# Performance work log

Hardware: AMD Instinct MI355X
Metric: run time of the kernel (lower is better)

The kernel has to match this reference:

```python
import jax, jax.numpy as jnp
import numpy as np

N = 100000   # nodes
E = 800000   # edges
H = 256      # hidden_dim == input_dim
L = 3        # num_layers
G = 64       # graphs in batch


def setup_inputs() -> dict:
    key = jax.random.key(0)
    ks = jax.random.split(key, 16)
    s = 0.05
    inp = {
        'x': jax.random.normal(ks[0], (N, H), jnp.float32),
        'edge_index': jax.random.randint(ks[1], (2, E), 0, N, dtype=jnp.int32),
        'batch': jnp.sort(jax.random.randint(ks[2], (N,), 0, G, dtype=jnp.int32)),
        'Ws': jax.random.normal(ks[3], (L, H, H), jnp.float32) * s,
        'Wn': jax.random.normal(ks[4], (L, H, H), jnp.float32) * s,
        'bs': jnp.zeros((L, H), jnp.float32),
        'att_w': jax.random.normal(ks[5], (H, 1), jnp.float32) * s,
        'att_b': jnp.zeros((1,), jnp.float32),
        'ne_W1': jax.random.normal(ks[6], (H, H // 2), jnp.float32) * s,
        'ne_b1': jnp.zeros((H // 2,), jnp.float32),
        'ne_W2': jax.random.normal(ks[7], (H // 2, 1), jnp.float32) * s,
        'ne_b2': jnp.zeros((1,), jnp.float32),
        'nd_W1': jax.random.normal(ks[8], (H, H // 2), jnp.float32) * s,
        'nd_b1': jnp.zeros((H // 2,), jnp.float32),
        'nd_W2': jax.random.normal(ks[9], (H // 2, 1), jnp.float32) * s,
        'nd_b2': jnp.zeros((1,), jnp.float32),
    }
    return inp


def reference(x, edge_index, batch, Ws, Wn, bs, att_w, att_b,
              ne_W1, ne_b1, ne_W2, ne_b2, nd_W1, nd_b1, nd_W2, nd_b2):
    src, dst = edge_index[0], edge_index[1]
    n = x.shape[0]
    # in-degree for mean aggregation (clamped to avoid div-by-zero)
    deg = jax.ops.segment_sum(jnp.ones(src.shape[0], x.dtype), dst, num_segments=n)
    deg = jnp.maximum(deg, 1.0)[:, None]                    # [N,1]
    # GNN encoder: SAGE-mean layers, ReLU (dropout identity at eval)
    h = x
    for l in range(Ws.shape[0]):
        msg = jax.ops.segment_sum(h[src], dst, num_segments=n) / deg  # [N,H]
        h = jax.nn.relu(h @ Ws[l] + msg @ Wn[l] + bs[l])
    # attention pooling: per-graph softmax over node scores
    s = (h @ att_w + att_b)[:, 0]                           # [N]
    m = jax.ops.segment_max(s, batch, num_segments=G)
    e = jnp.exp(s - m[batch])
    denom = jax.ops.segment_sum(e, batch, num_segments=G)
    alpha = (e / denom[batch])[:, None]                     # [N,1]
    g = jax.ops.segment_sum(alpha * h, batch, num_segments=G)  # [G,H]
    # heads: Linear-ReLU-(Dropout)-Linear
    graph_logits = jax.nn.relu(g @ ne_W1 + ne_b1) @ ne_W2 + ne_b2  # [G,1]
    node_logits = jax.nn.relu(h @ nd_W1 + nd_b1) @ nd_W2 + nd_b2  # [N,1]
    return (graph_logits, node_logits)
```

## Files before the change

### kernel.cpp

```cpp
#include <hip/hip_runtime.h>
#include <hip/hip_bf16.h>

#define HID 256
#define HHALF 128

typedef unsigned short u16;
typedef __attribute__((ext_vector_type(8))) short bf16x8;
typedef __attribute__((ext_vector_type(4))) float f32x4;

__device__ __forceinline__ float bf2f(unsigned int u) {
    unsigned int x = (u & 0xffffu) << 16;
    union { unsigned int i; float f; } c; c.i = x; return c.f;
}
__device__ __forceinline__ float lof(unsigned u) {
    union { unsigned i; float f; } c; c.i = u << 16; return c.f;
}
__device__ __forceinline__ float hif(unsigned u) {
    union { unsigned i; float f; } c; c.i = u & 0xffff0000u; return c.f;
}
__device__ __forceinline__ u16 f2bf(float f) {
    __hip_bfloat16 h = __float2bfloat16(f);
    union { __hip_bfloat16 h; u16 u; } c; c.h = h; return c.u;
}

__device__ __forceinline__ void gload16(const u16* g, u16* l) {
    __builtin_amdgcn_global_load_lds(
        (const __attribute__((address_space(1))) void*)g,
        (__attribute__((address_space(3))) void*)l, 16, 0, 0);
}

__global__ void k_count(const int* __restrict__ dst, int* __restrict__ cnt, int E) {
    int i = blockIdx.x * blockDim.x + threadIdx.x;
    if (i < E) atomicAdd(&cnt[dst[i]], 1);
}

__global__ void k_scan_block(const int* __restrict__ cnt, int* __restrict__ bsum, int n) {
    __shared__ int sd[256];
    int tid = threadIdx.x;
    int i = blockIdx.x * 256 + tid;
    int v = (i < n) ? cnt[i] : 0;
    sd[tid] = v; __syncthreads();
    for (int s = 128; s > 0; s >>= 1) {
        if (tid < s) sd[tid] += sd[tid + s];
        __syncthreads();
    }
    if (tid == 0) bsum[blockIdx.x] = sd[0];
}

__global__ void k_scan_top(int* __restrict__ bsum, int nb) {
    __shared__ int sd[512];
    int t = threadIdx.x;
    int v = (t < nb) ? bsum[t] : 0;
    sd[t] = v; __syncthreads();
    for (int s = 1; s < 512; s <<= 1) {
        int x = (t >= s) ? sd[t - s] : 0;
        __syncthreads();
        sd[t] += x;
        __syncthreads();
    }
    if (t < nb) bsum[t] = sd[t] - v;
}

__global__ void k_scan_down(const int* __restrict__ cnt, const int* __restrict__ boff,
                            int* __restrict__ row_off, int n, int total) {
    __shared__ int sd[256];
    int tid = threadIdx.x;
    int i = blockIdx.x * 256 + tid;
    int v = (i < n) ? cnt[i] : 0;
    sd[tid] = v; __syncthreads();
    for (int s = 1; s < 256; s <<= 1) {
        int x = (tid >= s) ? sd[tid - s] : 0;
        __syncthreads();
        sd[tid] += x;
        __syncthreads();
    }
    if (i < n) row_off[i] = boff[blockIdx.x] + sd[tid] - v;
    if (i == 0) row_off[n] = total;
}

__global__ void k_scatter(const int* __restrict__ src, const int* __restrict__ dst,
                          const int* __restrict__ row_off, int* __restrict__ fill,
                          int* __restrict__ col, int E) {
    int i = blockIdx.x * blockDim.x + threadIdx.x;
    if (i < E) {
        int d = dst[i];
        int p = atomicAdd(&fill[d], 1);
        col[row_off[d] + p] = src[i];
    }
}

__global__ void k_f2b(const float* __restrict__ in, u16* __restrict__ o, int total4) {
    int i = blockIdx.x * blockDim.x + threadIdx.x;
    if (i >= total4) return;
    float4 v = *(const float4*)&in[(size_t)i * 4];
    uint2 p;
    p.x = (unsigned)f2bf(v.x) | ((unsigned)f2bf(v.y) << 16);
    p.y = (unsigned)f2bf(v.z) | ((unsigned)f2bf(v.w) << 16);
    *(uint2*)&o[(size_t)i * 4] = p;
}

__global__ void k_wt_all(const float* __restrict__ Ws, const float* __restrict__ Wn,
                         const float* __restrict__ ndW1,
                         u16* __restrict__ WsT, u16* __restrict__ WnT,
                         u16* __restrict__ ndW1T, int L) {
    int idx = blockIdx.x * 256 + threadIdx.x;
    int mat = idx >> 16;
    int r = idx & 65535;
    int k = r >> 8, c = r & 255;
    if (mat < L) {
        WsT[(size_t)mat * 65536 + c * 256 + k] = f2bf(Ws[(size_t)mat * 65536 + k * 256 + c]);
    } else if (mat < 2 * L) {
        int l = mat - L;
        WnT[(size_t)l * 65536 + c * 256 + k] = f2bf(Wn[(size_t)l * 65536 + k * 256 + c]);
    } else {
        if (c < HHALF) ndW1T[c * 256 + k] = f2bf(ndW1[k * HHALF + c]);
    }
}

__global__ __launch_bounds__(256) void k_agg(
    const u16* __restrict__ h, const int* __restrict__ row_off,
    const int* __restrict__ col, u16* __restrict__ msg, int n) {
    int node = blockIdx.x * 4 + (threadIdx.x >> 6);
    if (node >= n) return;
    int lane = threadIdx.x & 63;
    int half = lane >> 5;
    int t = lane & 31;
    int s0 = row_off[node], s1 = row_off[node + 1];
    float a0 = 0.f, a1 = 0.f, a2 = 0.f, a3 = 0.f;
    float a4 = 0.f, a5 = 0.f, a6 = 0.f, a7 = 0.f;
    int e = s0;
    for (; e + 8 <= s1; e += 8) {
        int c0 = col[e + half];
        int c1 = col[e + 2 + half];
        int c2 = col[e + 4 + half];
        int c3 = col[e + 6 + half];
        uint4 v0 = *(const uint4*)&h[(size_t)c0 * HID + t * 8];
        uint4 v1 = *(const uint4*)&h[(size_t)c1 * HID + t * 8];
        uint4 v2 = *(const uint4*)&h[(size_t)c2 * HID + t * 8];
        uint4 v3 = *(const uint4*)&h[(size_t)c3 * HID + t * 8];
        a0 += (lof(v0.x) + lof(v1.x)) + (lof(v2.x) + lof(v3.x));
        a1 += (hif(v0.x) + hif(v1.x)) + (hif(v2.x) + hif(v3.x));
        a2 += (lof(v0.y) + lof(v1.y)) + (lof(v2.y) + lof(v3.y));
        a3 += (hif(v0.y) + hif(v1.y)) + (hif(v2.y) + hif(v3.y));
        a4 += (lof(v0.z) + lof(v1.z)) + (lof(v2.z) + lof(v3.z));
        a5 += (hif(v0.z) + hif(v1.z)) + (hif(v2.z) + hif(v3.z));
        a6 += (lof(v0.w) + lof(v1.w)) + (lof(v2.w) + lof(v3.w));
        a7 += (hif(v0.w) + hif(v1.w)) + (hif(v2.w) + hif(v3.w));
    }
    for (; e < s1; e += 2) {
        if (e + half < s1) {
            int c = col[e + half];
            uint4 v = *(const uint4*)&h[(size_t)c * HID + t * 8];
            a0 += lof(v.x); a1 += hif(v.x);
            a2 += lof(v.y); a3 += hif(v.y);
            a4 += lof(v.z); a5 += hif(v.z);
            a6 += lof(v.w); a7 += hif(v.w);
        }
    }
    a0 += __shfl_xor(a0, 32); a1 += __shfl_xor(a1, 32);
    a2 += __shfl_xor(a2, 32); a3 += __shfl_xor(a3, 32);
    a4 += __shfl_xor(a4, 32); a5 += __shfl_xor(a5, 32);
    a6 += __shfl_xor(a6, 32); a7 += __shfl_xor(a7, 32);
    if (half == 0) {
        int deg = s1 - s0;
        float inv = 1.0f / (float)(deg > 1 ? deg : 1);
        uint4 o;
        o.x = (unsigned)f2bf(a0 * inv) | ((unsigned)f2bf(a1 * inv) << 16);
        o.y = (unsigned)f2bf(a2 * inv) | ((unsigned)f2bf(a3 * inv) << 16);
        o.z = (unsigned)f2bf(a4 * inv) | ((unsigned)f2bf(a5 * inv) << 16);
        o.w = (unsigned)f2bf(a6 * inv) | ((unsigned)f2bf(a7 * inv) << 16);
        *(uint4*)&msg[(size_t)node * HID + t * 8] = o;
    }
}

__global__ __launch_bounds__(512) void k_gemm_bf(
    const u16* __restrict__ A1, const u16* __restrict__ W1t,
    const u16* __restrict__ A2, const u16* __restrict__ W2t,
    const float* __restrict__ bias, u16* __restrict__ out,
    int n, int ncols) {
    __shared__ __align__(16) u16 As[128 * 32];
    __shared__ __align__(16) u16 Bs[256 * 32];
    const int tid  = threadIdx.x;
    const int lane = tid & 63;
    const int w    = tid >> 6;
    const int wr   = w >> 2, wc = w & 3;
    const int brow = blockIdx.x * 128;
    const int nkt  = A2 ? 16 : 8;

    f32x4 acc[4][4];
    #pragma unroll
    for (int m = 0; m < 4; ++m)
        #pragma unroll
        for (int q = 0; q < 4; ++q)
            acc[m][q] = (f32x4){0.f, 0.f, 0.f, 0.f};

    const int arow_t = w * 16 + (lane >> 2);
    int arow = brow + arow_t; if (arow >= n) arow = n - 1;
    const int ach = (lane & 3) ^ ((arow_t >> 1) & 3);
    const size_t abase = (size_t)arow * HID + ach * 8;
    u16* As_dst = &As[(w * 16) * 32];

    const int brow0 = w * 32 + (lane >> 2);
    const int bch0  = (lane & 3) ^ ((brow0 >> 1) & 3);
    const size_t bbase0 = (size_t)brow0 * HID + bch0 * 8;
    u16* Bs_dst0 = &Bs[(w * 32) * 32];
    const int brow1 = brow0 + 16;
    const int bch1  = (lane & 3) ^ ((brow1 >> 1) & 3);
    const size_t bbase1 = (size_t)brow1 * HID + bch1 * 8;
    u16* Bs_dst1 = &Bs[(w * 32 + 16) * 32];

    const int lr = lane & 15;
    const int lq = lane >> 4;
    const int ph = lq ^ ((lr >> 1) & 3);

    for (int kt = 0; kt < nkt; ++kt) {
        const u16* A = (kt < 8) ? A1 : A2;
        const u16* W = (kt < 8) ? W1t : W2t;
        const int k0 = (kt & 7) * 32;
        __syncthreads();
        gload16(A + abase + k0, As_dst);
        gload16(W + bbase0 + k0, Bs_dst0);
        gload16(W + bbase1 + k0, Bs_dst1);
        __syncthreads();
        bf16x8 af[4], bg[4];
        #pragma unroll
        for (int m = 0; m < 4; ++m)
            af[m] = *(const bf16x8*)&As[(wr * 64 + m * 16 + lr) * 32 + ph * 8];
        #pragma unroll
        for (int q = 0; q < 4; ++q)
            bg[q] = *(const bf16x8*)&Bs[(wc * 64 + q * 16 + lr) * 32 + ph * 8];
        #pragma unroll
        for (int m = 0; m < 4; ++m)
            #pragma unroll
            for (int q = 0; q < 4; ++q)
                acc[m][q] = __builtin_amdgcn_mfma_f32_16x16x32_bf16(
                    bg[q], af[m], acc[m][q], 0, 0, 0);
    }

    #pragma unroll
    for (int m = 0; m < 4; ++m) {
        int row = brow + wr * 64 + m * 16 + lr;
        if (row >= n) continue;
        #pragma unroll
        for (int q = 0; q < 4; ++q) {
            int col = wc * 64 + q * 16 + lq * 4;
            if (col < ncols) {
                float4 bb = *(const float4*)&bias[col];
                uint2 o;
                o.x = (unsigned)f2bf(fmaxf(acc[m][q][0] + bb.x, 0.f))
                    | ((unsigned)f2bf(fmaxf(acc[m][q][1] + bb.y, 0.f)) << 16);
                o.y = (unsigned)f2bf(fmaxf(acc[m][q][2] + bb.z, 0.f))
                    | ((unsigned)f2bf(fmaxf(acc[m][q][3] + bb.w, 0.f)) << 16);
                *(uint2*)&out[(size_t)row * ncols + col] = o;
            }
        }
    }
}

__global__ void k_score(const u16* __restrict__ h, const float* __restrict__ att_w,
                        const float* __restrict__ att_b, float* __restrict__ s, int n) {
    int gw = (blockIdx.x * blockDim.x + threadIdx.x) >> 6;
    int lane = threadIdx.x & 63;
    if (gw >= n) return;
    uint2 v = *(const uint2*)&h[(size_t)gw * HID + lane * 4];
    float4 wv = *(const float4*)&att_w[lane * 4];
    float p = bf2f(v.x) * wv.x + bf2f(v.x >> 16) * wv.y
            + bf2f(v.y) * wv.z + bf2f(v.y >> 16) * wv.w;
    #pragma unroll
    for (int off = 32; off; off >>= 1) p += __shfl_xor(p, off, 64);
    if (lane == 0) s[gw] = p + att_b[0];
}

__global__ void k_gstart(const int* __restrict__ batch, int* __restrict__ gstart, int n, int G) {
    int i = blockIdx.x * blockDim.x + threadIdx.x;
    if (i >= n) return;
    int b = batch[i];
    int bp = (i == 0) ? -1 : batch[i - 1];
    for (int g = bp + 1; g <= b; ++g) gstart[g] = i;
    if (i == n - 1) {
        for (int g = b + 1; g <= G; ++g) gstart[g] = n;
    }
}

__global__ void k_mdenom(const float* __restrict__ s, const int* __restrict__ gstart,
                         float* __restrict__ m, float* __restrict__ denom) {
    int g = blockIdx.x;
    int t = threadIdx.x;
    int i0 = gstart[g], i1 = gstart[g + 1];
    __shared__ float red[256];
    float mx = -INFINITY;
    for (int i = i0 + t; i < i1; i += 256) mx = fmaxf(mx, s[i]);
    red[t] = mx; __syncthreads();
    for (int st = 128; st; st >>= 1) {
        if (t < st) red[t] = fmaxf(red[t], red[t + st]);
        __syncthreads();
    }
    float gm = red[0];
    __syncthreads();
    float sm = 0.f;
    for (int i = i0 + t; i < i1; i += 256) sm += expf(s[i] - gm);
    red[t] = sm; __syncthreads();
    for (int st = 128; st; st >>= 1) {
        if (t < st) red[t] += red[t + st];
        __syncthreads();
    }
    if (t == 0) { m[g] = gm; denom[g] = red[0]; }
}

__global__ void k_alpha(const float* __restrict__ s, const int* __restrict__ batch,
                        const float* __restrict__ m, const float* __restrict__ denom,
                        float* __restrict__ alpha, int n) {
    int i = blockIdx.x * blockDim.x + threadIdx.x;
    if (i >= n) return;
    int b = batch[i];
    float d = denom[b];
    alpha[i] = (d > 0.f) ? expf(s[i] - m[b]) / d : 0.f;
}

__global__ void k_pool(const u16* __restrict__ h, const float* __restrict__ alpha,
                       const int* __restrict__ gstart, float* __restrict__ gpool) {
    int g = blockIdx.x, sp = blockIdx.y, t = threadIdx.x;
    int i0 = gstart[g], i1 = gstart[g + 1];
    int len = i1 - i0;
    int a = i0 + (int)((long long)len * sp / 16);
    int b = i0 + (int)((long long)len * (sp + 1) / 16);
    float acc = 0.f;
    for (int i = a; i < b; ++i) acc += alpha[i] * bf2f(h[(size_t)i * HID + t]);
    if (acc != 0.f || sp == 0) atomicAdd(&gpool[g * HID + t], acc);
}

__global__ void k_ghead(const float* __restrict__ gpool, const float* __restrict__ W1,
                        const float* __restrict__ b1, const float* __restrict__ W2,
                        const float* __restrict__ b2, float* __restrict__ out) {
    int g = blockIdx.x, t = threadIdx.x;
    __shared__ float row[HID];
    __shared__ float red[128];
    row[t] = gpool[g * HID + t];
    row[t + 128] = gpool[g * HID + t + 128];
    __syncthreads();
    float acc = 0.f;
    #pragma unroll 8
    for (int k = 0; k < HID; ++k) acc = fmaf(row[k], W1[k * HHALF + t], acc);
    float hid = fmaxf(acc + b1[t], 0.f);
    red[t] = hid * W2[t];
    __syncthreads();
    for (int st = 64; st; st >>= 1) {
        if (t < st) red[t] += red[t + st];
        __syncthreads();
    }
    if (t == 0) out[g] = red[0] + b2[0];
}

__global__ void k_ndot(const u16* __restrict__ hid, const float* __restrict__ W2,
                       const float* __restrict__ b2, float* __restrict__ out, int n) {
    int gw = (blockIdx.x * blockDim.x + threadIdx.x) >> 6;
    int lane = threadIdx.x & 63;
    if (gw >= n) return;
    unsigned v = *(const unsigned*)&hid[(size_t)gw * HHALF + lane * 2];
    float val = bf2f(v) * W2[lane * 2] + bf2f(v >> 16) * W2[lane * 2 + 1];
    #pragma unroll
    for (int off = 32; off; off >>= 1) val += __shfl_xor(val, off, 64);
    if (lane == 0) out[gw] = val + b2[0];
}

extern "C" void kernel_launch(void* const* d_in, const int* in_sizes, int n_in,
                              void* d_out, int out_size, void* d_ws, size_t ws_size,
                              hipStream_t stream) {
    const float* x      = (const float*)d_in[0];
    const int*   eidx   = (const int*)d_in[1];
    const int*   batch  = (const int*)d_in[2];
    const float* Ws     = (const float*)d_in[3];
    const float* Wn     = (const float*)d_in[4];
    const float* bs     = (const float*)d_in[5];
    const float* att_w  = (const float*)d_in[6];
    const float* att_b  = (const float*)d_in[7];
    const float* ne_W1  = (const float*)d_in[8];
    const float* ne_b1  = (const float*)d_in[9];
    const float* ne_W2  = (const float*)d_in[10];
    const float* ne_b2  = (const float*)d_in[11];
    const float* nd_W1  = (const float*)d_in[12];
    const float* nd_b1  = (const float*)d_in[13];
    const float* nd_W2  = (const float*)d_in[14];
    const float* nd_b2  = (const float*)d_in[15];
    float* out = (float*)d_out;

    const int N = in_sizes[2];
    const int E = in_sizes[1] / 2;
    const int L = in_sizes[3] / (HID * HID);
    const int G = out_size - N;

    const int* src = eidx;
    const int* dst = eidx + E;

    size_t off = 0;
    auto alloc = [&](size_t bytes) {
        void* p = (char*)d_ws + off;
        off += (bytes + 255) & ~(size_t)255;
        return p;
    };
    int*   cnt     = (int*)alloc((size_t)N * 4);
    int*   row_off = (int*)alloc((size_t)(N + 1) * 4);
    int*   fill    = (int*)alloc((size_t)N * 4);
    int*   col     = (int*)alloc((size_t)E * 4);
    int*   gstart  = (int*)alloc((size_t)(G + 1) * 4);
    int*   bsum    = (int*)alloc(1024 * 4);
    float* sarr    = (float*)alloc((size_t)N * 4);
    float* alpha   = (float*)alloc((size_t)N * 4);
    float* marr    = (float*)alloc((size_t)G * 4);
    float* denom   = (float*)alloc((size_t)G * 4);
    float* gpool   = (float*)alloc((size_t)G * HID * 4);
    u16*   xb      = (u16*)alloc((size_t)N * HID * 2);
    u16*   msgb    = (u16*)alloc((size_t)N * HID * 2);
    u16*   hb1     = (u16*)alloc((size_t)N * HID * 2);
    u16*   hb2     = (u16*)alloc((size_t)N * HID * 2);
    u16*   hidb    = (u16*)alloc((size_t)N * HHALF * 2);
    u16*   WsT     = (u16*)alloc((size_t)L * HID * HID * 2);
    u16*   WnT     = (u16*)alloc((size_t)L * HID * HID * 2);
    u16*   ndW1T   = (u16*)alloc((size_t)HID * HID * 2);
    (void)ws_size;

    const int eb = (E + 255) / 256;
    const int nb = (N + 255) / 256;

    hipMemsetAsync(cnt, 0, (size_t)N * 4, stream);
    k_count<<<eb, 256, 0, stream>>>(dst, cnt, E);
    k_scan_block<<<nb, 256, 0, stream>>>(cnt, bsum, N);
    k_scan_top<<<1, 512, 0, stream>>>(bsum, nb);
    k_scan_down<<<nb, 256, 0, stream>>>(cnt, bsum, row_off, N, E);
    hipMemsetAsync(fill, 0, (size_t)N * 4, stream);
    k_scatter<<<eb, 256, 0, stream>>>(src, dst, row_off, fill, col, E);

    k_f2b<<<(N * HID / 4 + 255) / 256, 256, 0, stream>>>(x, xb, N * HID / 4);
    k_wt_all<<<(2 * L + 1) * (HID * HID / 256), 256, 0, stream>>>(
        Ws, Wn, nd_W1, WsT, WnT, ndW1T, L);

    const int gx = (N + 127) / 128;
    const u16* hin = xb;
    u16* hout = hb1;
    for (int l = 0; l < L; ++l) {
        k_agg<<<(N + 3) / 4, 256, 0, stream>>>(hin, row_off, col, msgb, N);
        k_gemm_bf<<<gx, 512, 0, stream>>>(
            hin, WsT + (size_t)l * HID * HID, msgb, WnT + (size_t)l * HID * HID,
            bs + (size_t)l * HID, hout, N, HID);
        hin = hout;
        hout = (hout == hb1) ? hb2 : hb1;
    }
    const u16* h = hin;

    k_score<<<(N + 3) / 4, 256, 0, stream>>>(h, att_w, att_b, sarr, N);
    k_gstart<<<nb, 256, 0, stream>>>(batch, gstart, N, G);
    k_mdenom<<<G, 256, 0, stream>>>(sarr, gstart, marr, denom);
    k_alpha<<<nb, 256, 0, stream>>>(sarr, batch, marr, denom, alpha, N);
    hipMemsetAsync(gpool, 0, (size_t)G * HID * 4, stream);
    k_pool<<<dim3(G, 16), HID, 0, stream>>>(h, alpha, gstart, gpool);

    k_ghead<<<G, HHALF, 0, stream>>>(gpool, ne_W1, ne_b1, ne_W2, ne_b2, out);

    k_gemm_bf<<<gx, 512, 0, stream>>>(
        h, ndW1T, nullptr, nullptr, nd_b1, hidb, N, HHALF);
    k_ndot<<<(N + 3) / 4, 256, 0, stream>>>(hidb, nd_W2, nd_b2, out + G, N);
}
```

Baseline: 588.7 us.

## Fuse score and node-head dot into GEMM epilogues, drop LDS staging

The attention-score dot product is folded into the epilogue of the last SAGE-layer GEMM, and the node-head second linear into the epilogue of the node-head GEMM, using atomicAdd on pre-zeroed outputs. This removes the k_score and k_ndot kernels and the hidden-activation buffer. Softmax alpha is now computed inside k_pool, so k_alpha is gone. The GEMM now loads MFMA fragments straight from global memory instead of staging them through LDS, and the aggregation tail is predicated and unrolled. Without LDS staging, waves that share rows re-read the same data and depend on the caches, which could slow the main GEMMs.

```diff
diff --git a/kernel.cpp b/kernel.cpp
--- a/kernel.cpp
+++ b/kernel.cpp
@@ -21,12 +21,6 @@
 __device__ __forceinline__ u16 f2bf(float f) {
     __hip_bfloat16 h = __float2bfloat16(f);
     union { __hip_bfloat16 h; u16 u; } c; c.h = h; return c.u;
-}
-
-__device__ __forceinline__ void gload16(const u16* g, u16* l) {
-    __builtin_amdgcn_global_load_lds(
-        (const __attribute__((address_space(1))) void*)g,
-        (__attribute__((address_space(3))) void*)l, 16, 0, 0);
 }
 
 __global__ void k_count(const int* __restrict__ dst, int* __restrict__ cnt, int E) {
@@ -147,15 +141,24 @@
         a6 += (lof(v0.w) + lof(v1.w)) + (lof(v2.w) + lof(v3.w));
         a7 += (hif(v0.w) + hif(v1.w)) + (hif(v2.w) + hif(v3.w));
     }
-    for (; e < s1; e += 2) {
-        if (e + half < s1) {
-            int c = col[e + half];
-            uint4 v = *(const uint4*)&h[(size_t)c * HID + t * 8];
-            a0 += lof(v.x); a1 += hif(v.x);
-            a2 += lof(v.y); a3 += hif(v.y);
-            a4 += lof(v.z); a5 += hif(v.z);
-            a6 += lof(v.w); a7 += hif(v.w);
-        }
+    if (e < s1) {
+        int i0 = e + half, i1 = e + 2 + half, i2 = e + 4 + half, i3 = e + 6 + half;
+        float w0 = (i0 < s1) ? 1.f : 0.f; int c0 = col[(i0 < s1) ? i0 : s0];
+        float w1 = (i1 < s1) ? 1.f : 0.f; int c1 = col[(i1 < s1) ? i1 : s0];
+        float w2 = (i2 < s1) ? 1.f : 0.f; int c2 = col[(i2 < s1) ? i2 : s0];
+        float w3 = (i3 < s1) ? 1.f : 0.f; int c3 = col[(i3 < s1) ? i3 : s0];
+        uint4 v0 = *(const uint4*)&h[(size_t)c0 * HID + t * 8];
+        uint4 v1 = *(const uint4*)&h[(size_t)c1 * HID + t * 8];
+        uint4 v2 = *(const uint4*)&h[(size_t)c2 * HID + t * 8];
+        uint4 v3 = *(const uint4*)&h[(size_t)c3 * HID + t * 8];
+        a0 = fmaf(w0, lof(v0.x), fmaf(w1, lof(v1.x), fmaf(w2, lof(v2.x), fmaf(w3, lof(v3.x), a0))));
+        a1 = fmaf(w0, hif(v0.x), fmaf(w1, hif(v1.x), fmaf(w2, hif(v2.x), fmaf(w3, hif(v3.x), a1))));
+        a2 = fmaf(w0, lof(v0.y), fmaf(w1, lof(v1.y), fmaf(w2, lof(v2.y), fmaf(w3, lof(v3.y), a2))));
+        a3 = fmaf(w0, hif(v0.y), fmaf(w1, hif(v1.y), fmaf(w2, hif(v2.y), fmaf(w3, hif(v3.y), a3))));
+        a4 = fmaf(w0, lof(v0.z), fmaf(w1, lof(v1.z), fmaf(w2, lof(v2.z), fmaf(w3, lof(v3.z), a4))));
+        a5 = fmaf(w0, hif(v0.z), fmaf(w1, hif(v1.z), fmaf(w2, hif(v2.z), fmaf(w3, hif(v3.z), a5))));
+        a6 = fmaf(w0, lof(v0.w), fmaf(w1, lof(v1.w), fmaf(w2, lof(v2.w), fmaf(w3, lof(v3.w), a6))));
+        a7 = fmaf(w0, hif(v0.w), fmaf(w1, hif(v1.w), fmaf(w2, hif(v2.w), fmaf(w3, hif(v3.w), a7))));
     }
     a0 += __shfl_xor(a0, 32); a1 += __shfl_xor(a1, 32);
     a2 += __shfl_xor(a2, 32); a3 += __shfl_xor(a3, 32);
@@ -177,15 +180,16 @@
     const u16* __restrict__ A1, const u16* __restrict__ W1t,
     const u16* __restrict__ A2, const u16* __restrict__ W2t,
     const float* __restrict__ bias, u16* __restrict__ out,
-    int n, int ncols) {
-    __shared__ __align__(16) u16 As[128 * 32];
-    __shared__ __align__(16) u16 Bs[256 * 32];
+    int n, int ncols,
+    const float* __restrict__ dotw, const float* __restrict__ dotb,
+    float* __restrict__ dotout) {
     const int tid  = threadIdx.x;
     const int lane = tid & 63;
     const int w    = tid >> 6;
     const int wr   = w >> 2, wc = w & 3;
     const int brow = blockIdx.x * 128;
-    const int nkt  = A2 ? 16 : 8;
+    const int lr = lane & 15;
+    const int lq = lane >> 4;
 
     f32x4 acc[4][4];
     #pragma unroll
@@ -194,81 +198,79 @@
         for (int q = 0; q < 4; ++q)
             acc[m][q] = (f32x4){0.f, 0.f, 0.f, 0.f};
 
-    const int arow_t = w * 16 + (lane >> 2);
-    int arow = brow + arow_t; if (arow >= n) arow = n - 1;
-    const int ach = (lane & 3) ^ ((arow_t >> 1) & 3);
-    const size_t abase = (size_t)arow * HID + ach * 8;
-    u16* As_dst = &As[(w * 16) * 32];
-
-    const int brow0 = w * 32 + (lane >> 2);
-    const int bch0  = (lane & 3) ^ ((brow0 >> 1) & 3);
-    const size_t bbase0 = (size_t)brow0 * HID + bch0 * 8;
-    u16* Bs_dst0 = &Bs[(w * 32) * 32];
-    const int brow1 = brow0 + 16;
-    const int bch1  = (lane & 3) ^ ((brow1 >> 1) & 3);
-    const size_t bbase1 = (size_t)brow1 * HID + bch1 * 8;
-    u16* Bs_dst1 = &Bs[(w * 32 + 16) * 32];
-
-    const int lr = lane & 15;
-    const int lq = lane >> 4;
-    const int ph = lq ^ ((lr >> 1) & 3);
-
-    for (int kt = 0; kt < nkt; ++kt) {
-        const u16* A = (kt < 8) ? A1 : A2;
-        const u16* W = (kt < 8) ? W1t : W2t;
-        const int k0 = (kt & 7) * 32;
-        __syncthreads();
-        gload16(A + abase + k0, As_dst);
-        gload16(W + bbase0 + k0, Bs_dst0);
-        gload16(W + bbase1 + k0, Bs_dst1);
-        __syncthreads();
-        bf16x8 af[4], bg[4];
+    size_t aoff[4];
+    #pragma unroll
+    for (int m = 0; m < 4; ++m) {
+        int r = brow + wr * 64 + m * 16 + lr;
+        if (r >= n) r = n - 1;
+        aoff[m] = (size_t)r * HID + lq * 8;
+    }
+    size_t boff[4];
+    #pragma unroll
+    for (int q = 0; q < 4; ++q) {
+        int c = wc * 64 + q * 16 + lr;
+        if (c >= ncols) c = ncols - 1;
+        boff[q] = (size_t)c * HID + lq * 8;
+    }
+
+    for (int ph = 0; ph < 2; ++ph) {
+        const u16* A = ph ? A2 : A1;
+        const u16* W = ph ? W2t : W1t;
+        if (!A) break;
         #pragma unroll
-        for (int m = 0; m < 4; ++m)
-            af[m] = *(const bf16x8*)&As[(wr * 64 + m * 16 + lr) * 32 + ph * 8];
-        #pragma unroll
-        for (int q = 0; q < 4; ++q)
-            bg[q] = *(const bf16x8*)&Bs[(wc * 64 + q * 16 + lr) * 32 + ph * 8];
-        #pragma unroll
-        for (int m = 0; m < 4; ++m)
+        for (int kt = 0; kt < 8; ++kt) {
+            const int k0 = kt * 32;
+            bf16x8 af[4], bg[4];
+            #pragma unroll
+            for (int m = 0; m < 4; ++m)
+                af[m] = *(const bf16x8*)(A + aoff[m] + k0);
             #pragma unroll
             for (int q = 0; q < 4; ++q)
-                acc[m][q] = __builtin_amdgcn_mfma_f32_16x16x32_bf16(
-                    bg[q], af[m], acc[m][q], 0, 0, 0);
+                bg[q] = *(const bf16x8*)(W + boff[q] + k0);
+            #pragma unroll
+            for (int m = 0; m < 4; ++m)
+                #pragma unroll
+                for (int q = 0; q < 4; ++q)
+                    acc[m][q] = __builtin_amdgcn_mfma_f32_16x16x32_bf16(
+                        bg[q], af[m], acc[m][q], 0, 0, 0);
+        }
     }
 
     #pragma unroll
     for (int m = 0; m < 4; ++m) {
         int row = brow + wr * 64 + m * 16 + lr;
         if (row >= n) continue;
+        float dpart = 0.f;
         #pragma unroll
         for (int q = 0; q < 4; ++q) {
             int col = wc * 64 + q * 16 + lq * 4;
             if (col < ncols) {
                 float4 bb = *(const float4*)&bias[col];
-                uint2 o;
-                o.x = (unsigned)f2bf(fmaxf(acc[m][q][0] + bb.x, 0.f))
-                    | ((unsigned)f2bf(fmaxf(acc[m][q][1] + bb.y, 0.f)) << 16);
-                o.y = (unsigned)f2bf(fmaxf(acc[m][q][2] + bb.z, 0.f))
-                    | ((unsigned)f2bf(fmaxf(acc[m][q][3] + bb.w, 0.f)) << 16);
-                *(uint2*)&out[(size_t)row * ncols + col] = o;
+                float r0 = fmaxf(acc[m][q][0] + bb.x, 0.f);
+                float r1 = fmaxf(acc[m][q][1] + bb.y, 0.f);
+                float r2 = fmaxf(acc[m][q][2] + bb.z, 0.f);
+                float r3 = fmaxf(acc[m][q][3] + bb.w, 0.f);
+                if (out) {
+                    uint2 o;
+                    o.x = (unsigned)f2bf(r0) | ((unsigned)f2bf(r1) << 16);
+                    o.y = (unsigned)f2bf(r2) | ((unsigned)f2bf(r3) << 16);
+                    *(uint2*)&out[(size_t)row * ncols + col] = o;
+                }
+                if (dotout) {
+                    float4 wv = *(const float4*)&dotw[col];
+                    dpart += r0 * wv.x + r1 * wv.y + r2 * wv.z + r3 * wv.w;
+                }
             }
         }
-    }
-}
-
-__global__ void k_score(const u16* __restrict__ h, const float* __restrict__ att_w,
-                        const float* __restrict__ att_b, float* __restrict__ s, int n) {
-    int gw = (blockIdx.x * blockDim.x + threadIdx.x) >> 6;
-    int lane = threadIdx.x & 63;
-    if (gw >= n) return;
-    uint2 v = *(const uint2*)&h[(size_t)gw * HID + lane * 4];
-    float4 wv = *(const float4*)&att_w[lane * 4];
-    float p = bf2f(v.x) * wv.x + bf2f(v.x >> 16) * wv.y
-            + bf2f(v.y) * wv.z + bf2f(v.y >> 16) * wv.w;
-    #pragma unroll
-    for (int off = 32; off; off >>= 1) p += __shfl_xor(p, off, 64);
-    if (lane == 0) s[gw] = p + att_b[0];
+        if (dotout && (wc * 64 < ncols)) {
+            dpart += __shfl_xor(dpart, 16);
+            dpart += __shfl_xor(dpart, 32);
+            if (lane < 16) {
+                float add = dpart + ((wc == 0) ? dotb[0] : 0.f);
+                atomicAdd(&dotout[row], add);
+            }
+        }
+    }
 }
 
 __global__ void k_gstart(const int* __restrict__ batch, int* __restrict__ gstart, int n, int G) {
@@ -307,25 +309,20 @@
     if (t == 0) { m[g] = gm; denom[g] = red[0]; }
 }
 
-__global__ void k_alpha(const float* __restrict__ s, const int* __restrict__ batch,
-                        const float* __restrict__ m, const float* __restrict__ denom,
-                        float* __restrict__ alpha, int n) {
-    int i = blockIdx.x * blockDim.x + threadIdx.x;
-    if (i >= n) return;
-    int b = batch[i];
-    float d = denom[b];
-    alpha[i] = (d > 0.f) ? expf(s[i] - m[b]) / d : 0.f;
-}
-
-__global__ void k_pool(const u16* __restrict__ h, const float* __restrict__ alpha,
+__global__ void k_pool(const u16* __restrict__ h, const float* __restrict__ sarr,
+                       const float* __restrict__ marr, const float* __restrict__ denom,
                        const int* __restrict__ gstart, float* __restrict__ gpool) {
     int g = blockIdx.x, sp = blockIdx.y, t = threadIdx.x;
     int i0 = gstart[g], i1 = gstart[g + 1];
     int len = i1 - i0;
     int a = i0 + (int)((long long)len * sp / 16);
     int b = i0 + (int)((long long)len * (sp + 1) / 16);
+    float dn = denom[g];
+    float inv = (dn > 0.f) ? 1.0f / dn : 0.f;
+    float mg = marr[g];
     float acc = 0.f;
-    for (int i = a; i < b; ++i) acc += alpha[i] * bf2f(h[(size_t)i * HID + t]);
+    for (int i = a; i < b; ++i)
+        acc += expf(sarr[i] - mg) * inv * bf2f(h[(size_t)i * HID + t]);
     if (acc != 0.f || sp == 0) atomicAdd(&gpool[g * HID + t], acc);
 }
 
@@ -349,18 +346,6 @@
         __syncthreads();
     }
     if (t == 0) out[g] = red[0] + b2[0];
-}
-
-__global__ void k_ndot(const u16* __restrict__ hid, const float* __restrict__ W2,
-                       const float* __restrict__ b2, float* __restrict__ out, int n) {
-    int gw = (blockIdx.x * blockDim.x + threadIdx.x) >> 6;
-    int lane = threadIdx.x & 63;
-    if (gw >= n) return;
-    unsigned v = *(const unsigned*)&hid[(size_t)gw * HHALF + lane * 2];
-    float val = bf2f(v) * W2[lane * 2] + bf2f(v >> 16) * W2[lane * 2 + 1];
-    #pragma unroll
-    for (int off = 32; off; off >>= 1) val += __shfl_xor(val, off, 64);
-    if (lane == 0) out[gw] = val + b2[0];
 }
 
 extern "C" void kernel_launch(void* const* d_in, const int* in_sizes, int n_in,
@@ -405,7 +390,6 @@
     int*   gstart  = (int*)alloc((size_t)(G + 1) * 4);
     int*   bsum    = (int*)alloc(1024 * 4);
     float* sarr    = (float*)alloc((size_t)N * 4);
-    float* alpha   = (float*)alloc((size_t)N * 4);
     float* marr    = (float*)alloc((size_t)G * 4);
     float* denom   = (float*)alloc((size_t)G * 4);
     float* gpool   = (float*)alloc((size_t)G * HID * 4);
@@ -413,7 +397,6 @@
     u16*   msgb    = (u16*)alloc((size_t)N * HID * 2);
     u16*   hb1     = (u16*)alloc((size_t)N * HID * 2);
     u16*   hb2     = (u16*)alloc((size_t)N * HID * 2);
-    u16*   hidb    = (u16*)alloc((size_t)N * HHALF * 2);
     u16*   WsT     = (u16*)alloc((size_t)L * HID * HID * 2);
     u16*   WnT     = (u16*)alloc((size_t)L * HID * HID * 2);
     u16*   ndW1T   = (u16*)alloc((size_t)HID * HID * 2);
@@ -434,29 +417,32 @@
     k_wt_all<<<(2 * L + 1) * (HID * HID / 256), 256, 0, stream>>>(
         Ws, Wn, nd_W1, WsT, WnT, ndW1T, L);
 
+    hipMemsetAsync(sarr, 0, (size_t)N * 4, stream);
+    hipMemsetAsync(out + G, 0, (size_t)N * 4, stream);
+
     const int gx = (N + 127) / 128;
     const u16* hin = xb;
     u16* hout = hb1;
     for (int l = 0; l < L; ++l) {
+        bool last = (l == L - 1);
         k_agg<<<(N + 3) / 4, 256, 0, stream>>>(hin, row_off, col, msgb, N);
         k_gemm_bf<<<gx, 512, 0, stream>>>(
             hin, WsT + (size_t)l * HID * HID, msgb, WnT + (size_t)l * HID * HID,
-            bs + (size_t)l * HID, hout, N, HID);
+            bs + (size_t)l * HID, hout, N, HID,
+            last ? att_w : nullptr, last ? att_b : nullptr, last ? sarr : nullptr);
         hin = hout;
         hout = (hout == hb1) ? hb2 : hb1;
     }
     const u16* h = hin;
 
-    k_score<<<(N + 3) / 4, 256, 0, stream>>>(h, att_w, att_b, sarr, N);
     k_gstart<<<nb, 256, 0, stream>>>(batch, gstart, N, G);
     k_mdenom<<<G, 256, 0, stream>>>(sarr, gstart, marr, denom);
-    k_alpha<<<nb, 256, 0, stream>>>(sarr, batch, marr, denom, alpha, N);
     hipMemsetAsync(gpool, 0, (size_t)G * HID * 4, stream);
-    k_pool<<<dim3(G, 16), HID, 0, stream>>>(h, alpha, gstart, gpool);
+    k_pool<<<dim3(G, 16), HID, 0, stream>>>(h, sarr, marr, denom, gstart, gpool);
 
     k_ghead<<<G, HHALF, 0, stream>>>(gpool, ne_W1, ne_b1, ne_W2, ne_b2, out);
 
     k_gemm_bf<<<gx, 512, 0, stream>>>(
-        h, ndW1T, nullptr, nullptr, nd_b1, hidb, N, HHALF);
-    k_ndot<<<(N + 3) / 4, 256, 0, stream>>>(hidb, nd_W2, nd_b2, out + G, N);
-}
+        h, ndW1T, nullptr, nullptr, nd_b1, nullptr, N, HHALF,
+        nd_W2, nd_b2, out + G);
+}
```

New measurement: 825.1 us. 40.2% more time.
